# Optimization experiments

Hardware: AMD Instinct MI355X
Metric: run time of the kernel (lower is better)

The kernel has to match this reference:

```python
import jax, jax.numpy as jnp
import numpy as np

NEG_SLOPE = 0.01


def _pos(x):
    return jnp.where(x > 0, x, jnp.zeros_like(x))


def _neg(x):
    return jnp.where(x < 0, x, jnp.zeros_like(x))


def setup_inputs() -> dict:
    N = 4096
    key = jax.random.key(0)
    k1, k2, k3, k4, k5, k6 = jax.random.split(key, 6)
    x = jax.random.normal(k1, (1, N), dtype=jnp.float32)
    eps = 0.1
    lb0 = x - eps
    ub0 = x + eps
    scale = 1.0 / np.sqrt(N)
    W1 = jax.random.normal(k2, (N, N), dtype=jnp.float32) * scale
    b1 = jax.random.normal(k3, (1, N), dtype=jnp.float32)
    W2 = jax.random.normal(k4, (N, N), dtype=jnp.float32) * scale
    b2 = jax.random.normal(k5, (1, N), dtype=jnp.float32)
    raw_alpha = jax.random.normal(k6, (N,), dtype=jnp.float32)
    return {"lb0": lb0, "ub0": ub0, "W1": W1, "b1": b1, "W2": W2, "b2": b2, "raw_alpha": raw_alpha}


def reference(lb0, ub0, W1, b1, W2, b2, raw_alpha):
    N = raw_alpha.shape[0]
    ns = NEG_SLOPE
    # ---- backsubstitution: fold layer2 transformer through layer1 (affine: lslope=uslope=W1) ----
    clslope, clintercept, cuslope, cuintercept = W2, b2, W2, b2
    clp, cln = _pos(clslope), _neg(clslope)
    cup, cun = _pos(cuslope), _neg(cuslope)
    clintercept = b1 @ clp.T + b1 @ cln.T + clintercept  # [1,N]
    cuintercept = b1 @ cup.T + b1 @ cun.T + cuintercept
    clslope = clp @ W1 + cln @ W1  # [N,N]
    cuslope = cup @ W1 + cun @ W1
    # ---- certifier against initial interval bounds ----
    lsp, lsn = _pos(clslope), _neg(clslope)
    usp, usn = _pos(cuslope), _neg(cuslope)
    lbounds = lb0 @ lsp.T + ub0 @ lsn.T + clintercept  # [1,N]
    ubounds = ub0 @ usp.T + lb0 @ usn.T + cuintercept
    # ---- DeepPoly LeakyReLU relaxation (neg_slope <= 1 branch) ----
    alpha = jax.nn.sigmoid(raw_alpha)
    slope = ((ubounds - lbounds * ns) / (ubounds - lbounds)).reshape(-1)  # [N]
    slope = jnp.where(jnp.isnan(slope), jnp.zeros_like(slope), slope)
    intercept = (1.0 - slope) * ubounds  # [1,N]
    ones = jnp.ones((N,), dtype=lbounds.dtype)
    zeros_row = jnp.zeros((1, N), dtype=lbounds.dtype)
    lslope, lintercept = ones, zeros_row
    uslope, uintercept = ones, zeros_row
    below = (ubounds <= 0).reshape(-1)
    above = (lbounds >= 0).reshape(-1)
    lslope = jnp.where(below, ns * ones, lslope)
    uslope = jnp.where(below, ns * ones, uslope)
    lslope = jnp.where(above, ones, lslope)
    uslope = jnp.where(above, ones, uslope)
    crossing = ~(below | above)
    uslope = jnp.where(crossing, slope, uslope)
    uintercept = jnp.where(crossing, intercept, uintercept)
    lslope_v1 = jnp.where(crossing, ones, lslope)
    lslope_v2 = jnp.where(crossing, ns * ones, lslope)
    lslope = alpha * lslope_v1 + (1.0 - alpha) * lslope_v2
    return jnp.diag(lslope), lintercept, jnp.diag(uslope), uintercept
```

## Files before the change

### kernel.cpp

```cpp
#include <hip/hip_runtime.h>
#include <stdint.h>

#define NN 4096
#define NEG_SLOPE 0.01f

typedef _Float16 f16x8 __attribute__((ext_vector_type(8)));
typedef _Float16 f16x4 __attribute__((ext_vector_type(4)));
typedef float f32x4 __attribute__((ext_vector_type(4)));

#define L_DIAG 0
#define L_INT  16777216
#define U_DIAG 16781312
#define U_INT  33558528
#define TAIL0  33554432

__device__ __forceinline__ void async_ld16(void* lds, const void* g) {
    __builtin_amdgcn_global_load_lds(
        (__attribute__((address_space(1))) const void*)(const void*)g,
        (__attribute__((address_space(3))) void*)lds, 16, 0, 0);
}

__global__ __launch_bounds__(256, 4)
void gemm_SU(const _Float16* __restrict__ Ah, const _Float16* __restrict__ Bt,
             const float* __restrict__ lb0, const float* __restrict__ ub0,
             float* __restrict__ S, float* __restrict__ U,
             f32x4* __restrict__ zbase) {
    __shared__ _Float16 sA[128][64];
    __shared__ _Float16 sB[128][64];
    const int t = threadIdx.x;
    const int lane = t & 63;
    const int w = t >> 6;
    const int waveRow = w >> 1, waveCol = w & 1;
    const int quad = lane >> 4, l15 = lane & 15, l7 = lane & 7;

    const int bRow = (blockIdx.x >> 5) * 128;
    const int bCol = (blockIdx.x & 31) * 128;

    const int rOff = lane >> 3;
    const int uG   = (lane & 7) ^ (lane >> 3);
    const _Float16* gA = Ah + (size_t)(bRow + w * 32 + rOff) * NN + uG * 8;
    const _Float16* gB = Bt + (size_t)(bCol + w * 32 + rOff) * NN + uG * 8;

    f32x4 acc[4][4];
#pragma unroll
    for (int i = 0; i < 4; ++i)
#pragma unroll
        for (int j = 0; j < 4; ++j) acc[i][j] = (f32x4){0.f, 0.f, 0.f, 0.f};

    const f32x4 zv = (f32x4){0.f, 0.f, 0.f, 0.f};

    for (int kt = 0; kt < NN / 64; ++kt) {
        const int k0 = kt * 64;
        __syncthreads();
#pragma unroll
        for (int i = 0; i < 4; ++i) {
            async_ld16(&sA[w * 32 + i * 8][0], gA + (size_t)(i * 8) * NN + k0);
            async_ld16(&sB[w * 32 + i * 8][0], gB + (size_t)(i * 8) * NN + k0);
        }
        __syncthreads();

#pragma unroll
        for (int s = 0; s < 2; ++s) {
            f16x8 af[4];
#pragma unroll
            for (int fr = 0; fr < 4; ++fr) {
                const int r = waveRow * 64 + fr * 16 + l15;
                af[fr] = *(const f16x8*)&sA[r][((s * 4 + quad) ^ l7) * 8];
            }
#pragma unroll
            for (int fc = 0; fc < 4; ++fc) {
                const int c = waveCol * 64 + fc * 16 + l15;
                const f16x8 bf = *(const f16x8*)&sB[c][((s * 4 + quad) ^ l7) * 8];
#pragma unroll
                for (int fr = 0; fr < 4; ++fr)
                    acc[fr][fc] = __builtin_amdgcn_mfma_f32_16x16x32_f16(af[fr], bf, acc[fr][fc], 0, 0, 0);
            }
        }

        if ((kt & 3) == 0) {
            const int zi = kt >> 2;
            __builtin_nontemporal_store(zv,
                zbase + (size_t)blockIdx.x * 4096 + zi * 256 + t);
        }
    }

    float ev[4], cv[4];
#pragma unroll
    for (int fc = 0; fc < 4; ++fc) {
        const int col = bCol + waveCol * 64 + fc * 16 + l15;
        const float l = lb0[col], u_ = ub0[col];
        ev[fc] = 0.5f * (u_ - l);
        cv[fc] = 0.5f * (u_ + l);
    }
#pragma unroll
    for (int fr = 0; fr < 4; ++fr) {
#pragma unroll
        for (int r = 0; r < 4; ++r) {
            float sv = 0.f, uv = 0.f;
#pragma unroll
            for (int fc = 0; fc < 4; ++fc) {
                const float m = acc[fr][fc][r];
                sv += ev[fc] * fabsf(m);
                uv += cv[fc] * m;
            }
#pragma unroll
            for (int mk = 1; mk < 16; mk <<= 1) {
                sv += __shfl_xor(sv, mk, 64);
                uv += __shfl_xor(uv, mk, 64);
            }
            if (l15 == 0) {
                const int row = bRow + waveRow * 64 + fr * 16 + quad * 4 + r;
                atomicAdd(&S[row], sv);
                atomicAdd(&U[row], uv);
            }
        }
    }
}

__global__ __launch_bounds__(256)
void prep(const float* __restrict__ W2, const float* __restrict__ W1,
          const float* __restrict__ b1, const float* __restrict__ b2,
          _Float16* __restrict__ Ah, _Float16* __restrict__ Bt,
          float* __restrict__ cj, float* __restrict__ S, float* __restrict__ U) {
    __shared__ float sT[64][65];
    __shared__ float w4[4];
    const int b = blockIdx.x;
    const int t = threadIdx.x;
    if (b < 4096) {
        const int j = b;
        const float* row = W2 + (size_t)j * NN;
        _Float16* orow = Ah + (size_t)j * NN;
        float d1 = 0.f;
#pragma unroll
        for (int p = 0; p < 4; ++p) {
            const int i = p * 1024 + t * 4;
            const float4 a = *(const float4*)&row[i];
            const float4 bb = *(const float4*)&b1[i];
            d1 += a.x * bb.x + a.y * bb.y + a.z * bb.z + a.w * bb.w;
            f16x4 h;
            h[0] = (_Float16)a.x; h[1] = (_Float16)a.y;
            h[2] = (_Float16)a.z; h[3] = (_Float16)a.w;
            *(f16x4*)&orow[i] = h;
        }
#pragma unroll
        for (int mk = 1; mk < 64; mk <<= 1) d1 += __shfl_xor(d1, mk, 64);
        if ((t & 63) == 0) w4[t >> 6] = d1;
        __syncthreads();
        if (t == 0) {
            cj[j] = w4[0] + w4[1] + w4[2] + w4[3] + b2[j];
            S[j] = 0.f;
            U[j] = 0.f;
        }
    } else {
        const int tile = b - 4096;
        const int bi = (tile & 63) * 64;
        const int bn = (tile >> 6) * 64;
        const int r = t >> 4, c4 = (t & 15) * 4;
#pragma unroll
        for (int p = 0; p < 4; ++p) {
            const float4 a = *(const float4*)&W1[(size_t)(bi + r + p * 16) * NN + bn + c4];
            sT[r + p * 16][c4 + 0] = a.x;
            sT[r + p * 16][c4 + 1] = a.y;
            sT[r + p * 16][c4 + 2] = a.z;
            sT[r + p * 16][c4 + 3] = a.w;
        }
        __syncthreads();
        const int n = t >> 4, k4 = (t & 15) * 4;
#pragma unroll
        for (int p = 0; p < 4; ++p) {
            const int nn_ = n + p * 16;
            f16x4 h;
            h[0] = (_Float16)sT[k4 + 0][nn_];
            h[1] = (_Float16)sT[k4 + 1][nn_];
            h[2] = (_Float16)sT[k4 + 2][nn_];
            h[3] = (_Float16)sT[k4 + 3][nn_];
            *(f16x4*)&Bt[(size_t)(bn + nn_) * NN + bi + k4] = h;
        }
    }
}

__device__ __forceinline__ void get_lub(int j, const float* S, const float* U,
                                        const float* cj, float& lb, float& ub) {
    const float base = U[j] + cj[j], Sv = S[j];
    lb = base - Sv;
    ub = base + Sv;
}
__device__ __forceinline__ float slope_of(float lb, float ub) {
    float s = (ub - lb * NEG_SLOPE) / (ub - lb);
    if (!(s == s)) s = 0.f;
    return s;
}
__device__ __forceinline__ float uslope_of(float lb, float ub) {
    const bool below = (ub <= 0.f), above = (lb >= 0.f);
    return (!(below || above)) ? slope_of(lb, ub) : (below ? NEG_SLOPE : 1.f);
}

__global__ __launch_bounds__(256)
void finish(const float* __restrict__ S, const float* __restrict__ U,
            const float* __restrict__ cj, const float* __restrict__ ra,
            float* __restrict__ out) {
    const int b = blockIdx.x;
    const int t = threadIdx.x;
    if (b < 4096) {
        const int j = b;
        float lb, ub;
        get_lub(j, S, U, cj, lb, ub);
        const float alpha = 1.f / (1.f + expf(-ra[j]));
        const bool below = (ub <= 0.f), above = (lb >= 0.f);
        const bool crossing = !(below || above);
        const float v1 = below ? NEG_SLOPE : 1.f;
        const float v2 = crossing ? NEG_SLOPE : v1;
        const float lslope = alpha * v1 + (1.f - alpha) * v2;
        f32x4* rowp = (f32x4*)(out + (size_t)j * NN);
        const int dq = j >> 2, dr = j & 3;
#pragma unroll
        for (int q = 0; q < 4; ++q) {
            const int i4 = t + q * 256;
            f32x4 z = (f32x4){0.f, 0.f, 0.f, 0.f};
            if (i4 == dq) z[dr] = lslope;
            __builtin_nontemporal_store(z, &rowp[i4]);
        }
    } else if (b < 4112) {
        const int j = (b - 4096) * 256 + t;
        if (j < 4095) {
            float lb, ub;
            get_lub(j, S, U, cj, lb, ub);
            out[U_DIAG + (size_t)j * NN + j] = uslope_of(lb, ub);
        }
    } else if (b == 4112) {
        f32x4* p = (f32x4*)(out + TAIL0);
#pragma unroll
        for (int q = 0; q < 4; ++q) {
            const int i4 = t + q * 256;
            f32x4 z = (f32x4){0.f, 0.f, 0.f, 0.f};
            if (i4 == 1023) {
                float lb, ub;
                get_lub(4095, S, U, cj, lb, ub);
                z[3] = uslope_of(lb, ub);
            }
            __builtin_nontemporal_store(z, &p[i4]);
        }
    } else {
#pragma unroll
        for (int q = 0; q < 16; ++q) {
            const int j = t + q * 256;
            float lb, ub;
            get_lub(j, S, U, cj, lb, ub);
            const bool below = (ub <= 0.f), above = (lb >= 0.f);
            const bool crossing = !(below || above);
            out[U_INT + j] = crossing ? (1.f - slope_of(lb, ub)) * ub : 0.f;
        }
    }
}

extern "C" void kernel_launch(void* const* d_in, const int* in_sizes, int n_in,
                              void* d_out, int out_size, void* d_ws, size_t ws_size,
                              hipStream_t stream) {
    const float* lb0 = (const float*)d_in[0];
    const float* ub0 = (const float*)d_in[1];
    const float* W1  = (const float*)d_in[2];
    const float* b1  = (const float*)d_in[3];
    const float* W2  = (const float*)d_in[4];
    const float* b2  = (const float*)d_in[5];
    const float* ra  = (const float*)d_in[6];
    float* out = (float*)d_out;

    _Float16* Ah = (_Float16*)d_out;
    _Float16* Bt = Ah + (size_t)NN * NN;

    float* S  = (float*)d_ws;
    float* U  = S + NN;
    float* cj = U + NN;

    prep<<<dim3(8192), dim3(256), 0, stream>>>(W2, W1, b1, b2, Ah, Bt, cj, S, U);
    gemm_SU<<<dim3(1024), dim3(256), 0, stream>>>(Ah, Bt, lb0, ub0, S, U,
                                                  (f32x4*)(out + L_INT));
    finish<<<dim3(4114), dim3(256), 0, stream>>>(S, U, cj, ra, out);
}
```

Before: 379.2 us.

## Stage fp16 operands in workspace and zero both output diagonals inside GEMM

When the workspace is large enough, the fp16 copies of W2 and transposed W1 go into the workspace instead of the output buffer. The GEMM kernel's interleaved zero-stores then clear the whole first 64 MB of the output, not only the region after the first diagonal matrix. The finish kernel shrinks to 18 blocks that write only the diagonal elements, upper intercepts and the tail, which removes a separate full-matrix zero-fill pass. The prep kernel also uses 8-wide fp16 stores. The old path is kept as a fallback when the workspace is too small.

```diff
diff --git a/kernel.cpp b/kernel.cpp
--- a/kernel.cpp
+++ b/kernel.cpp
@@ -8,11 +8,11 @@
 typedef _Float16 f16x4 __attribute__((ext_vector_type(4)));
 typedef float f32x4 __attribute__((ext_vector_type(4)));
 
-#define L_DIAG 0
 #define L_INT  16777216
 #define U_DIAG 16781312
 #define U_INT  33558528
 #define TAIL0  33554432
+#define TAIL2  33554432
 
 __device__ __forceinline__ void async_ld16(void* lds, const void* g) {
     __builtin_amdgcn_global_load_lds(
@@ -20,6 +20,7 @@
         (__attribute__((address_space(3))) void*)lds, 16, 0, 0);
 }
 
+template<int EVERY>
 __global__ __launch_bounds__(256, 4)
 void gemm_SU(const _Float16* __restrict__ Ah, const _Float16* __restrict__ Bt,
              const float* __restrict__ lb0, const float* __restrict__ ub0,
@@ -48,6 +49,7 @@
         for (int j = 0; j < 4; ++j) acc[i][j] = (f32x4){0.f, 0.f, 0.f, 0.f};
 
     const f32x4 zv = (f32x4){0.f, 0.f, 0.f, 0.f};
+    const int NZB = (64 / EVERY) * 256;
 
     for (int kt = 0; kt < NN / 64; ++kt) {
         const int k0 = kt * 64;
@@ -77,10 +79,10 @@
             }
         }
 
-        if ((kt & 3) == 0) {
-            const int zi = kt >> 2;
+        if ((kt & (EVERY - 1)) == 0) {
+            const int zi = kt / EVERY;
             __builtin_nontemporal_store(zv,
-                zbase + (size_t)blockIdx.x * 4096 + zi * 256 + t);
+                zbase + (size_t)blockIdx.x * NZB + zi * 256 + t);
         }
     }
 
@@ -132,15 +134,20 @@
         _Float16* orow = Ah + (size_t)j * NN;
         float d1 = 0.f;
 #pragma unroll
-        for (int p = 0; p < 4; ++p) {
-            const int i = p * 1024 + t * 4;
-            const float4 a = *(const float4*)&row[i];
-            const float4 bb = *(const float4*)&b1[i];
-            d1 += a.x * bb.x + a.y * bb.y + a.z * bb.z + a.w * bb.w;
-            f16x4 h;
-            h[0] = (_Float16)a.x; h[1] = (_Float16)a.y;
-            h[2] = (_Float16)a.z; h[3] = (_Float16)a.w;
-            *(f16x4*)&orow[i] = h;
+        for (int p = 0; p < 2; ++p) {
+            const int i = p * 2048 + t * 8;
+            const float4 a0 = *(const float4*)&row[i];
+            const float4 a1 = *(const float4*)&row[i + 4];
+            const float4 b0 = *(const float4*)&b1[i];
+            const float4 b1v = *(const float4*)&b1[i + 4];
+            d1 += a0.x * b0.x + a0.y * b0.y + a0.z * b0.z + a0.w * b0.w;
+            d1 += a1.x * b1v.x + a1.y * b1v.y + a1.z * b1v.z + a1.w * b1v.w;
+            f16x8 h;
+            h[0] = (_Float16)a0.x; h[1] = (_Float16)a0.y;
+            h[2] = (_Float16)a0.z; h[3] = (_Float16)a0.w;
+            h[4] = (_Float16)a1.x; h[5] = (_Float16)a1.y;
+            h[6] = (_Float16)a1.z; h[7] = (_Float16)a1.w;
+            *(f16x8*)&orow[i] = h;
         }
 #pragma unroll
         for (int mk = 1; mk < 64; mk <<= 1) d1 += __shfl_xor(d1, mk, 64);
@@ -165,16 +172,14 @@
             sT[r + p * 16][c4 + 3] = a.w;
         }
         __syncthreads();
-        const int n = t >> 4, k4 = (t & 15) * 4;
-#pragma unroll
-        for (int p = 0; p < 4; ++p) {
-            const int nn_ = n + p * 16;
-            f16x4 h;
-            h[0] = (_Float16)sT[k4 + 0][nn_];
-            h[1] = (_Float16)sT[k4 + 1][nn_];
-            h[2] = (_Float16)sT[k4 + 2][nn_];
-            h[3] = (_Float16)sT[k4 + 3][nn_];
-            *(f16x4*)&Bt[(size_t)(bn + nn_) * NN + bi + k4] = h;
+        const int k8 = (t & 7) * 8;
+#pragma unroll
+        for (int p = 0; p < 2; ++p) {
+            const int n = (t >> 3) + p * 32;
+            f16x8 h;
+#pragma unroll
+            for (int e = 0; e < 8; ++e) h[e] = (_Float16)sT[k8 + e][n];
+            *(f16x8*)&Bt[(size_t)(bn + n) * NN + bi + k8] = h;
         }
     }
 }
@@ -194,30 +199,72 @@
     const bool below = (ub <= 0.f), above = (lb >= 0.f);
     return (!(below || above)) ? slope_of(lb, ub) : (below ? NEG_SLOPE : 1.f);
 }
+__device__ __forceinline__ float lslope_of(float lb, float ub, float raw) {
+    const float alpha = 1.f / (1.f + expf(-raw));
+    const bool below = (ub <= 0.f), above = (lb >= 0.f);
+    const bool crossing = !(below || above);
+    const float v1 = below ? NEG_SLOPE : 1.f;
+    const float v2 = crossing ? NEG_SLOPE : v1;
+    return alpha * v1 + (1.f - alpha) * v2;
+}
 
 __global__ __launch_bounds__(256)
-void finish(const float* __restrict__ S, const float* __restrict__ U,
-            const float* __restrict__ cj, const float* __restrict__ ra,
-            float* __restrict__ out) {
+void finish_fast(const float* __restrict__ S, const float* __restrict__ U,
+                 const float* __restrict__ cj, const float* __restrict__ ra,
+                 float* __restrict__ out) {
+    const int b = blockIdx.x;
+    const int t = threadIdx.x;
+    if (b == 0) {
+        f32x4* p = (f32x4*)(out + TAIL2);
+#pragma unroll
+        for (int q = 0; q < 4; ++q) {
+            const int i4 = t + q * 256;
+            f32x4 z = (f32x4){0.f, 0.f, 0.f, 0.f};
+            if (i4 == 1023) {
+                float lb, ub;
+                get_lub(4095, S, U, cj, lb, ub);
+                z[3] = uslope_of(lb, ub);
+            }
+            __builtin_nontemporal_store(z, &p[i4]);
+        }
+    } else if (b <= 16) {
+        const int j = (b - 1) * 256 + t;
+        float lb, ub;
+        get_lub(j, S, U, cj, lb, ub);
+        out[(size_t)j * (NN + 1)] = lslope_of(lb, ub, ra[j]);
+        if (j < 4095)
+            out[U_DIAG + (size_t)j * (NN + 1)] = uslope_of(lb, ub);
+    } else {
+#pragma unroll
+        for (int q = 0; q < 16; ++q) {
+            const int j = t + q * 256;
+            float lb, ub;
+            get_lub(j, S, U, cj, lb, ub);
+            const bool below = (ub <= 0.f), above = (lb >= 0.f);
+            const bool crossing = !(below || above);
+            out[U_INT + j] = crossing ? (1.f - slope_of(lb, ub)) * ub : 0.f;
+        }
+    }
+}
+
+__global__ __launch_bounds__(256)
+void finish_slow(const float* __restrict__ S, const float* __restrict__ U,
+                 const float* __restrict__ cj, const float* __restrict__ ra,
+                 float* __restrict__ out) {
     const int b = blockIdx.x;
     const int t = threadIdx.x;
     if (b < 4096) {
         const int j = b;
         float lb, ub;
         get_lub(j, S, U, cj, lb, ub);
-        const float alpha = 1.f / (1.f + expf(-ra[j]));
-        const bool below = (ub <= 0.f), above = (lb >= 0.f);
-        const bool crossing = !(below || above);
-        const float v1 = below ? NEG_SLOPE : 1.f;
-        const float v2 = crossing ? NEG_SLOPE : v1;
-        const float lslope = alpha * v1 + (1.f - alpha) * v2;
+        const float ls = lslope_of(lb, ub, ra[j]);
         f32x4* rowp = (f32x4*)(out + (size_t)j * NN);
         const int dq = j >> 2, dr = j & 3;
 #pragma unroll
         for (int q = 0; q < 4; ++q) {
             const int i4 = t + q * 256;
             f32x4 z = (f32x4){0.f, 0.f, 0.f, 0.f};
-            if (i4 == dq) z[dr] = lslope;
+            if (i4 == dq) z[dr] = ls;
             __builtin_nontemporal_store(z, &rowp[i4]);
         }
     } else if (b < 4112) {
@@ -265,15 +312,27 @@
     const float* ra  = (const float*)d_in[6];
     float* out = (float*)d_out;
 
-    _Float16* Ah = (_Float16*)d_out;
-    _Float16* Bt = Ah + (size_t)NN * NN;
-
     float* S  = (float*)d_ws;
     float* U  = S + NN;
     float* cj = U + NN;
 
-    prep<<<dim3(8192), dim3(256), 0, stream>>>(W2, W1, b1, b2, Ah, Bt, cj, S, U);
-    gemm_SU<<<dim3(1024), dim3(256), 0, stream>>>(Ah, Bt, lb0, ub0, S, U,
-                                                  (f32x4*)(out + L_INT));
-    finish<<<dim3(4114), dim3(256), 0, stream>>>(S, U, cj, ra, out);
-}
+    const size_t need = 3 * (size_t)NN * sizeof(float)
+                      + 2 * (size_t)NN * NN * sizeof(_Float16);
+    const bool fast = ws_size >= need;
+
+    if (fast) {
+        _Float16* Ah = (_Float16*)(cj + NN);
+        _Float16* Bt = Ah + (size_t)NN * NN;
+        prep<<<dim3(8192), dim3(256), 0, stream>>>(W2, W1, b1, b2, Ah, Bt, cj, S, U);
+        gemm_SU<2><<<dim3(1024), dim3(256), 0, stream>>>(Ah, Bt, lb0, ub0, S, U,
+                                                         (f32x4*)out);
+        finish_fast<<<dim3(18), dim3(256), 0, stream>>>(S, U, cj, ra, out);
+    } else {
+        _Float16* Ah = (_Float16*)d_out;
+        _Float16* Bt = Ah + (size_t)NN * NN;
+        prep<<<dim3(8192), dim3(256), 0, stream>>>(W2, W1, b1, b2, Ah, Bt, cj, S, U);
+        gemm_SU<4><<<dim3(1024), dim3(256), 0, stream>>>(Ah, Bt, lb0, ub0, S, U,
+                                                         (f32x4*)(out + L_INT));
+        finish_slow<<<dim3(4114), dim3(256), 0, stream>>>(S, U, cj, ra, out);
+    }
+}
```

New measurement: 374.9 us. Within noise of the previous version (-1.1%).
